# Kernel tuning notes

Measured on AMD Instinct MI355X. Metric: run time of the kernel, lower is better.

The kernel has to match this reference:

```python
import jax, jax.numpy as jnp
import numpy as np

N_NODES = 50000
N_EDGES = 800000
GNN_IN, GNN_HID, GNN_OUT = 64, 128, 64
MLP_HID, MLP_OUT = 128, 1
EDGE_DIST_DIM = 16
NEG_SLOPE = 0.2


def setup_inputs() -> dict:
    key = jax.random.key(0)
    ks = jax.random.split(key, 16)
    inp = {
        "x": jax.random.normal(ks[0], (N_NODES, GNN_IN), dtype=jnp.float32),
        "edge_index": jax.random.randint(ks[1], (N_EDGES, 2), 0, N_NODES, dtype=jnp.int32),
        "edge_dist": jax.random.normal(ks[2], (N_EDGES, EDGE_DIST_DIM), dtype=jnp.float32),
        # GATConv layer 1
        "W_g1": jax.random.normal(ks[3], (GNN_IN, GNN_HID), dtype=jnp.float32) / np.sqrt(GNN_IN),
        "a1_src": jax.random.normal(ks[4], (GNN_HID,), dtype=jnp.float32) / np.sqrt(GNN_HID),
        "a1_dst": jax.random.normal(ks[5], (GNN_HID,), dtype=jnp.float32) / np.sqrt(GNN_HID),
        "b_g1": jnp.zeros((GNN_HID,), dtype=jnp.float32),
        # GATConv layer 2
        "W_g2": jax.random.normal(ks[6], (GNN_HID, GNN_OUT), dtype=jnp.float32) / np.sqrt(GNN_HID),
        "a2_src": jax.random.normal(ks[7], (GNN_OUT,), dtype=jnp.float32) / np.sqrt(GNN_OUT),
        "a2_dst": jax.random.normal(ks[8], (GNN_OUT,), dtype=jnp.float32) / np.sqrt(GNN_OUT),
        "b_g2": jnp.zeros((GNN_OUT,), dtype=jnp.float32),
        # edge MLP: in = (GNN_IN + GNN_OUT)*2 + EDGE_DIST_DIM = 272
        "W_m1": jax.random.normal(ks[9], ((GNN_IN + GNN_OUT) * 2 + EDGE_DIST_DIM, MLP_HID), dtype=jnp.float32) / np.sqrt((GNN_IN + GNN_OUT) * 2 + EDGE_DIST_DIM),
        "b_m1": jnp.zeros((MLP_HID,), dtype=jnp.float32),
        "W_m2": jax.random.normal(ks[10], (MLP_HID, MLP_OUT), dtype=jnp.float32) / np.sqrt(MLP_HID),
        "b_m2": jnp.zeros((MLP_OUT,), dtype=jnp.float32),
    }
    return inp


def gat_conv(x, src, dst, W, a_src, a_dst, bias, n_nodes):
    """Single-head GATConv (PyG defaults: self-loops already included in src/dst)."""
    h = x @ W                                # (N, out)
    alpha_s = h @ a_src                      # (N,)
    alpha_d = h @ a_dst                      # (N,)
    e = jax.nn.leaky_relu(alpha_s[src] + alpha_d[dst], NEG_SLOPE)  # (E,)
    # segment softmax over incoming edges of each destination node
    e_max = jax.ops.segment_max(e, dst, num_segments=n_nodes)
    w = jnp.exp(e - e_max[dst])
    denom = jax.ops.segment_sum(w, dst, num_segments=n_nodes)
    alpha = w / (denom[dst] + 1e-16)
    out = jax.ops.segment_sum(alpha[:, None] * h[src], dst, num_segments=n_nodes)
    return out + bias


def reference(x, edge_index, edge_dist,
              W_g1, a1_src, a1_dst, b_g1,
              W_g2, a2_src, a2_dst, b_g2,
              W_m1, b_m1, W_m2, b_m2):
    n = x.shape[0]
    row = edge_index[:, 0]
    col = edge_index[:, 1]
    # undirected edges + self loops (PyG GATConv add_self_loops=True)
    loops = jnp.arange(n, dtype=edge_index.dtype)
    src = jnp.concatenate([row, col, loops])
    dst = jnp.concatenate([col, row, loops])

    f = jax.nn.relu(gat_conv(x, src, dst, W_g1, a1_src, a1_dst, b_g1, n))
    f = jax.nn.relu(gat_conv(f, src, dst, W_g2, a2_src, a2_dst, b_g2, n))

    xf = jnp.concatenate([x, f], axis=1)     # (N, gnn_in+gnn_out)
    edge_attr = jnp.concatenate([xf[row], xf[col], edge_dist], axis=1)  # (E, 272)
    h = jax.nn.relu(edge_attr @ W_m1 + b_m1)
    return jax.nn.sigmoid(h @ W_m2 + b_m2)   # (E, 1)
```

## Files before the change

### kernel.cpp

```cpp
#include <hip/hip_runtime.h>
#include <hip/hip_bf16.h>
#include <math.h>


#define GIN 64
#define GHID 128
#define GOUT 64

typedef unsigned int u32;
typedef unsigned short u16;

__device__ __forceinline__ float bflo(u32 u) {
  union { u32 i; float f; } c; c.i = u << 16; return c.f;
}
__device__ __forceinline__ float bfhi(u32 u) {
  union { u32 i; float f; } c; c.i = u & 0xffff0000u; return c.f;
}
__device__ __forceinline__ u16 f2bf(float x) {
  __hip_bfloat16 h = __float2bfloat16(x);
  return *reinterpret_cast<u16*>(&h);
}


__global__ void hist_kernel(const int* __restrict__ eidx, int* __restrict__ deg,
                            int nE, int n) {
  int tot = 2 * nE + n;
  for (int i = blockIdx.x * blockDim.x + threadIdx.x; i < tot;
       i += gridDim.x * blockDim.x) {
    int dst;
    if (i < nE) dst = eidx[2 * i + 1];
    else if (i < 2 * nE) dst = eidx[2 * (i - nE)];
    else dst = i - 2 * nE;
    atomicAdd(&deg[dst], 1);
  }
}

#define SCAN_CHUNK 1024
__global__ void scan_partial(const int* __restrict__ deg, int* __restrict__ bsum,
                             int n) {
  int b = blockIdx.x, tid = threadIdx.x;
  int base = b * SCAN_CHUNK + tid * 4;
  int s = 0;
#pragma unroll
  for (int c = 0; c < 4; ++c) { int i = base + c; if (i < n) s += deg[i]; }
#pragma unroll
  for (int off = 32; off; off >>= 1) s += __shfl_xor(s, off, 64);
  __shared__ int ws[4];
  if ((tid & 63) == 0) ws[tid >> 6] = s;
  __syncthreads();
  if (tid == 0) bsum[b] = ws[0] + ws[1] + ws[2] + ws[3];
}
__global__ void scan_bsums(const int* __restrict__ bsum, int* __restrict__ bscan,
                           int* __restrict__ offs, int nb, int n) {
  int lane = threadIdx.x;
  int v = (lane < nb) ? bsum[lane] : 0;
  int incl = v;
#pragma unroll
  for (int off = 1; off < 64; off <<= 1) {
    int t = __shfl_up(incl, off, 64);
    if (lane >= off) incl += t;
  }
  if (lane < nb) bscan[lane] = incl - v;
  if (lane == 63) offs[n] = incl;
}
__global__ void scan_final(const int* __restrict__ deg, const int* __restrict__ bscan,
                           int* __restrict__ offs, int* __restrict__ cursor, int n) {
  int b = blockIdx.x, tid = threadIdx.x;
  int base = b * SCAN_CHUNK + tid * 4;
  int v[4]; int s = 0;
#pragma unroll
  for (int c = 0; c < 4; ++c) { int i = base + c; v[c] = (i < n) ? deg[i] : 0; s += v[c]; }
  int lane = tid & 63, wv = tid >> 6;
  int incl = s;
#pragma unroll
  for (int off = 1; off < 64; off <<= 1) {
    int t = __shfl_up(incl, off, 64);
    if (lane >= off) incl += t;
  }
  __shared__ int ws[4];
  if (lane == 63) ws[wv] = incl;
  __syncthreads();
  int woff = 0;
  for (int w2 = 0; w2 < wv; ++w2) woff += ws[w2];
  int excl = bscan[b] + woff + incl - s;
#pragma unroll
  for (int c = 0; c < 4; ++c) {
    int i = base + c;
    if (i < n) { offs[i] = excl; cursor[i] = excl; }
    excl += v[c];
  }
}

__global__ void scatter_kernel(const int* __restrict__ eidx, int* __restrict__ cursor,
                               int* __restrict__ csr, int nE, int n) {
  int tot = 2 * nE + n;
  for (int i = blockIdx.x * blockDim.x + threadIdx.x; i < tot;
       i += gridDim.x * blockDim.x) {
    int src, dst;
    if (i < nE)          { src = eidx[2 * i];            dst = eidx[2 * i + 1]; }
    else if (i < 2 * nE) { src = eidx[2 * (i - nE) + 1]; dst = eidx[2 * (i - nE)]; }
    else                 { src = i - 2 * nE;             dst = src; }
    int pos = atomicAdd(&cursor[dst], 1);
    csr[pos] = src;
  }
}


template <bool SCORES>
__global__ __launch_bounds__(256) void gemm_bf(
    const float* __restrict__ A, const float* __restrict__ A2, int ksp,
    int lda, int lda2,
    const float* __restrict__ B, int bskip, int ldb,
    u16* __restrict__ Cb, int ldcb,
    const float* __restrict__ av, const float* __restrict__ bv,
    float* __restrict__ as_, float* __restrict__ ad_,
    int M, int K) {
  __shared__ float As[32][68];
  __shared__ float Bs[32][64];
  int tid = threadIdx.x;
  int m0 = blockIdx.x * 64;
  int n0 = blockIdx.y * 64;
  const float* Bp = B + (size_t)(n0 >> 7) * bskip;
  int nb0 = n0 & 127;
  int tx = tid & 15, ty = tid >> 4;
  float acc[4][4] = {};
  for (int k0 = 0; k0 < K; k0 += 32) {
    const float* Asrc; int Alda; int kk;
    if (k0 < ksp) { Asrc = A;  Alda = lda;  kk = k0; }
    else          { Asrc = A2; Alda = lda2; kk = k0 - ksp; }
#pragma unroll
    for (int r = 0; r < 2; ++r) {
      int m = (tid >> 3) + r * 32;
      int k = (tid & 7) * 4;
      float4 v = make_float4(0.f, 0.f, 0.f, 0.f);
      int gm = m0 + m;
      if (gm < M) v = *reinterpret_cast<const float4*>(&Asrc[(size_t)gm * Alda + kk + k]);
      As[k + 0][m] = v.x; As[k + 1][m] = v.y; As[k + 2][m] = v.z; As[k + 3][m] = v.w;
    }
#pragma unroll
    for (int r = 0; r < 2; ++r) {
      int k = (tid >> 4) + r * 16;
      int nn = (tid & 15) * 4;
      float4 v = *reinterpret_cast<const float4*>(&Bp[(size_t)(k0 + k) * ldb + nb0 + nn]);
      *reinterpret_cast<float4*>(&Bs[k][nn]) = v;
    }
    __syncthreads();
#pragma unroll
    for (int k = 0; k < 32; ++k) {
      float a[4], b[4];
#pragma unroll
      for (int i = 0; i < 4; ++i) a[i] = As[k][ty * 4 + i];
#pragma unroll
      for (int i = 0; i < 4; ++i) b[i] = Bs[k][tx * 4 + i];
#pragma unroll
      for (int i = 0; i < 4; ++i)
#pragma unroll
        for (int j = 0; j < 4; ++j) acc[i][j] += a[i] * b[j];
    }
    __syncthreads();
  }
  float avv[4], bvv[4];
  if constexpr (SCORES) {
#pragma unroll
    for (int j = 0; j < 4; ++j) {
      avv[j] = av[n0 + tx * 4 + j];
      bvv[j] = bv[n0 + tx * 4 + j];
    }
  }
#pragma unroll
  for (int i = 0; i < 4; ++i) {
    int gm = m0 + ty * 4 + i;
    bool inb = gm < M;
    if (inb) {
      u16* bp = &Cb[(size_t)gm * ldcb + n0 + tx * 4];
      *reinterpret_cast<ushort4*>(bp) = make_ushort4(
          f2bf(acc[i][0]), f2bf(acc[i][1]), f2bf(acc[i][2]), f2bf(acc[i][3]));
    }
    if constexpr (SCORES) {
      float ps = acc[i][0] * avv[0] + acc[i][1] * avv[1] +
                 acc[i][2] * avv[2] + acc[i][3] * avv[3];
      float pd = acc[i][0] * bvv[0] + acc[i][1] * bvv[1] +
                 acc[i][2] * bvv[2] + acc[i][3] * bvv[3];
#pragma unroll
      for (int off = 1; off < 16; off <<= 1) {
        ps += __shfl_xor(ps, off, 16);
        pd += __shfl_xor(pd, off, 16);
      }
      if (tx == 0 && inb) {
        atomicAdd(&as_[gm], ps);
        atomicAdd(&ad_[gm], pd);
      }
    }
  }
}


__global__ __launch_bounds__(256) void gat_agg1(
    const u16* __restrict__ hb, const float* __restrict__ as_,
    const float* __restrict__ ad_, const int* __restrict__ offs,
    const int* __restrict__ csr, const float* __restrict__ bias,
    float* __restrict__ out, int n) {
  int node = blockIdx.x * 4 + (threadIdx.x >> 6);
  if (node >= n) return;
  int lane = threadIdx.x & 63;
  int g = lane >> 3, sl = lane & 7;
  int beg = offs[node], end = offs[node + 1];
  float adn = ad_[node];
  float denom = 0.f;
  float a[16] = {};
  int i0 = beg + g;
  int s0 = (i0 < end) ? csr[i0] : -1;
  uint4 pa0 = make_uint4(0,0,0,0), pb0 = make_uint4(0,0,0,0); float e0 = 0.f;
  if (s0 >= 0) {
    const u16* row = &hb[(size_t)s0 * 128 + sl * 16];
    pa0 = *reinterpret_cast<const uint4*>(row);
    pb0 = *reinterpret_cast<const uint4*>(row + 8);
    e0 = as_[s0] + adn;
  }
  int i1 = i0 + 8;
  int s1 = (i1 < end) ? csr[i1] : -1;
  while (s0 >= 0) {
    int i2 = i1 + 8;
    int s2 = (i2 < end) ? csr[i2] : -1;
    uint4 pa1 = make_uint4(0,0,0,0), pb1 = make_uint4(0,0,0,0); float e1 = 0.f;
    if (s1 >= 0) {
      const u16* row = &hb[(size_t)s1 * 128 + sl * 16];
      pa1 = *reinterpret_cast<const uint4*>(row);
      pb1 = *reinterpret_cast<const uint4*>(row + 8);
      e1 = as_[s1] + adn;
    }
    float e = (e0 > 0.f) ? e0 : 0.2f * e0;
    float wgt = __expf(e);
    denom += wgt;
    a[0]  += wgt * bflo(pa0.x); a[1]  += wgt * bfhi(pa0.x);
    a[2]  += wgt * bflo(pa0.y); a[3]  += wgt * bfhi(pa0.y);
    a[4]  += wgt * bflo(pa0.z); a[5]  += wgt * bfhi(pa0.z);
    a[6]  += wgt * bflo(pa0.w); a[7]  += wgt * bfhi(pa0.w);
    a[8]  += wgt * bflo(pb0.x); a[9]  += wgt * bfhi(pb0.x);
    a[10] += wgt * bflo(pb0.y); a[11] += wgt * bfhi(pb0.y);
    a[12] += wgt * bflo(pb0.z); a[13] += wgt * bfhi(pb0.z);
    a[14] += wgt * bflo(pb0.w); a[15] += wgt * bfhi(pb0.w);
    s0 = s1; pa0 = pa1; pb0 = pb1; e0 = e1;
    s1 = s2; i1 = i2;
  }
  denom += __shfl_xor(denom, 8, 64);
  denom += __shfl_xor(denom, 16, 64);
  denom += __shfl_xor(denom, 32, 64);
#pragma unroll
  for (int j = 0; j < 16; ++j) {
    a[j] += __shfl_xor(a[j], 8, 64);
    a[j] += __shfl_xor(a[j], 16, 64);
    a[j] += __shfl_xor(a[j], 32, 64);
  }
  if (g == 0) {
    float inv = 1.f / (denom + 1e-16f);
    float* op = &out[(size_t)node * 128 + sl * 16];
    const float* bp = &bias[sl * 16];
#pragma unroll
    for (int q = 0; q < 4; ++q) {
      float4 bq = *reinterpret_cast<const float4*>(bp + q * 4);
      float4 o;
      o.x = fmaxf(a[q * 4 + 0] * inv + bq.x, 0.f);
      o.y = fmaxf(a[q * 4 + 1] * inv + bq.y, 0.f);
      o.z = fmaxf(a[q * 4 + 2] * inv + bq.z, 0.f);
      o.w = fmaxf(a[q * 4 + 3] * inv + bq.w, 0.f);
      *reinterpret_cast<float4*>(op + q * 4) = o;
    }
  }
}


__global__ __launch_bounds__(256) void gat_agg2(
    const u16* __restrict__ hb, const float* __restrict__ as_,
    const float* __restrict__ ad_, const int* __restrict__ offs,
    const int* __restrict__ csr, const float* __restrict__ bias,
    float* __restrict__ out, int n) {
  int node = blockIdx.x * 4 + (threadIdx.x >> 6);
  if (node >= n) return;
  int lane = threadIdx.x & 63;
  int g = lane >> 2, sl = lane & 3;
  int beg = offs[node], end = offs[node + 1];
  float adn = ad_[node];
  float denom = 0.f;
  float a[16] = {};
  int i0 = beg + g;
  int s0 = (i0 < end) ? csr[i0] : -1;
  uint4 pa0 = make_uint4(0,0,0,0), pb0 = make_uint4(0,0,0,0); float e0 = 0.f;
  if (s0 >= 0) {
    const u16* row = &hb[(size_t)s0 * 64 + sl * 16];
    pa0 = *reinterpret_cast<const uint4*>(row);
    pb0 = *reinterpret_cast<const uint4*>(row + 8);
    e0 = as_[s0] + adn;
  }
  int i1 = i0 + 16;
  int s1 = (i1 < end) ? csr[i1] : -1;
  while (s0 >= 0) {
    int i2 = i1 + 16;
    int s2 = (i2 < end) ? csr[i2] : -1;
    uint4 pa1 = make_uint4(0,0,0,0), pb1 = make_uint4(0,0,0,0); float e1 = 0.f;
    if (s1 >= 0) {
      const u16* row = &hb[(size_t)s1 * 64 + sl * 16];
      pa1 = *reinterpret_cast<const uint4*>(row);
      pb1 = *reinterpret_cast<const uint4*>(row + 8);
      e1 = as_[s1] + adn;
    }
    float e = (e0 > 0.f) ? e0 : 0.2f * e0;
    float wgt = __expf(e);
    denom += wgt;
    a[0]  += wgt * bflo(pa0.x); a[1]  += wgt * bfhi(pa0.x);
    a[2]  += wgt * bflo(pa0.y); a[3]  += wgt * bfhi(pa0.y);
    a[4]  += wgt * bflo(pa0.z); a[5]  += wgt * bfhi(pa0.z);
    a[6]  += wgt * bflo(pa0.w); a[7]  += wgt * bfhi(pa0.w);
    a[8]  += wgt * bflo(pb0.x); a[9]  += wgt * bfhi(pb0.x);
    a[10] += wgt * bflo(pb0.y); a[11] += wgt * bfhi(pb0.y);
    a[12] += wgt * bflo(pb0.z); a[13] += wgt * bfhi(pb0.z);
    a[14] += wgt * bflo(pb0.w); a[15] += wgt * bfhi(pb0.w);
    s0 = s1; pa0 = pa1; pb0 = pb1; e0 = e1;
    s1 = s2; i1 = i2;
  }
#pragma unroll
  for (int w2 = 4; w2 < 64; w2 <<= 1) denom += __shfl_xor(denom, w2, 64);
#pragma unroll
  for (int j = 0; j < 16; ++j) {
    a[j] += __shfl_xor(a[j], 4, 64);
    a[j] += __shfl_xor(a[j], 8, 64);
    a[j] += __shfl_xor(a[j], 16, 64);
    a[j] += __shfl_xor(a[j], 32, 64);
  }
  if (g == 0) {
    float inv = 1.f / (denom + 1e-16f);
    float* op = &out[(size_t)node * 64 + sl * 16];
    const float* bp = &bias[sl * 16];
#pragma unroll
    for (int q = 0; q < 4; ++q) {
      float4 bq = *reinterpret_cast<const float4*>(bp + q * 4);
      float4 o;
      o.x = fmaxf(a[q * 4 + 0] * inv + bq.x, 0.f);
      o.y = fmaxf(a[q * 4 + 1] * inv + bq.y, 0.f);
      o.z = fmaxf(a[q * 4 + 2] * inv + bq.z, 0.f);
      o.w = fmaxf(a[q * 4 + 3] * inv + bq.w, 0.f);
      *reinterpret_cast<float4*>(op + q * 4) = o;
    }
  }
}


__global__ __launch_bounds__(256) void edge_mlp(
    const int2* __restrict__ eidx, const float* __restrict__ dist,
    const u16* __restrict__ Pb, const float* __restrict__ W3,
    const float* __restrict__ b1, const float* __restrict__ W2,
    const float* __restrict__ b2, float* __restrict__ out, int nE) {
  __shared__ float4 W3s[16][32];
  int tid = threadIdx.x;
  for (int idx = tid; idx < 16 * 32; idx += 256) {
    int k = idx >> 5, q = idx & 31;
    W3s[k][q] = *reinterpret_cast<const float4*>(&W3[k * 128 + q * 4]);
  }
  __syncthreads();
  int lane = tid & 63, wv = tid >> 6;
  int g = lane >> 4, sl = lane & 15;
  float4 b1a = *reinterpret_cast<const float4*>(&b1[sl * 8]);
  float4 b1b = *reinterpret_cast<const float4*>(&b1[sl * 8 + 4]);
  float4 w2a = *reinterpret_cast<const float4*>(&W2[sl * 8]);
  float4 w2b = *reinterpret_cast<const float4*>(&W2[sl * 8 + 4]);
  float b2v = b2[0];
  const int stride = gridDim.x * 16;
  int e0 = (blockIdx.x * 4 + wv) * 4 + g;
  bool v0 = e0 < nE;
  int2 rc0 = v0 ? eidx[e0] : make_int2(0, 0);
  uint4 p1 = make_uint4(0,0,0,0), p2 = make_uint4(0,0,0,0); float ds0 = 0.f;
  if (v0) {
    p1 = *reinterpret_cast<const uint4*>(&Pb[(size_t)rc0.x * 256 + sl * 8]);
    p2 = *reinterpret_cast<const uint4*>(&Pb[(size_t)rc0.y * 256 + 128 + sl * 8]);
    ds0 = dist[(size_t)e0 * 16 + sl];
  }
  int e1 = e0 + stride;
  bool v1 = e1 < nE;
  int2 rc1 = v1 ? eidx[e1] : make_int2(0, 0);
  while (v0) {
    int e2 = e1 + stride;
    bool v2 = e2 < nE;
    int2 rc2 = v2 ? eidx[e2] : make_int2(0, 0);
    uint4 q1 = make_uint4(0,0,0,0), q2 = make_uint4(0,0,0,0); float ds1 = 0.f;
    if (v1) {
      q1 = *reinterpret_cast<const uint4*>(&Pb[(size_t)rc1.x * 256 + sl * 8]);
      q2 = *reinterpret_cast<const uint4*>(&Pb[(size_t)rc1.y * 256 + 128 + sl * 8]);
      ds1 = dist[(size_t)e1 * 16 + sl];
    }
    float a[8];
    a[0] = bflo(p1.x) + bflo(p2.x) + b1a.x;
    a[1] = bfhi(p1.x) + bfhi(p2.x) + b1a.y;
    a[2] = bflo(p1.y) + bflo(p2.y) + b1a.z;
    a[3] = bfhi(p1.y) + bfhi(p2.y) + b1a.w;
    a[4] = bflo(p1.z) + bflo(p2.z) + b1b.x;
    a[5] = bfhi(p1.z) + bfhi(p2.z) + b1b.y;
    a[6] = bflo(p1.w) + bflo(p2.w) + b1b.z;
    a[7] = bfhi(p1.w) + bfhi(p2.w) + b1b.w;
#pragma unroll
    for (int k = 0; k < 16; ++k) {
      float dk = __shfl(ds0, (g << 4) + k, 64);
      float4 wA = W3s[k][2 * sl];
      float4 wB = W3s[k][2 * sl + 1];
      a[0] += dk * wA.x; a[1] += dk * wA.y; a[2] += dk * wA.z; a[3] += dk * wA.w;
      a[4] += dk * wB.x; a[5] += dk * wB.y; a[6] += dk * wB.z; a[7] += dk * wB.w;
    }
    float p_ = fmaxf(a[0], 0.f) * w2a.x + fmaxf(a[1], 0.f) * w2a.y +
               fmaxf(a[2], 0.f) * w2a.z + fmaxf(a[3], 0.f) * w2a.w +
               fmaxf(a[4], 0.f) * w2b.x + fmaxf(a[5], 0.f) * w2b.y +
               fmaxf(a[6], 0.f) * w2b.z + fmaxf(a[7], 0.f) * w2b.w;
#pragma unroll
    for (int off = 1; off < 16; off <<= 1) p_ += __shfl_xor(p_, off, 16);
    if (sl == 0) out[e0] = 1.f / (1.f + __expf(-(p_ + b2v)));
    e0 = e1; v0 = v1; p1 = q1; p2 = q2; ds0 = ds1;
    e1 = e2; v1 = v2; rc1 = rc2;
  }
}


extern "C" void kernel_launch(void* const* d_in, const int* in_sizes, int n_in,
                              void* d_out, int out_size, void* d_ws, size_t ws_size,
                              hipStream_t stream) {
  const float* x      = (const float*)d_in[0];
  const int*   eidx   = (const int*)d_in[1];
  const float* dist   = (const float*)d_in[2];
  const float* W_g1   = (const float*)d_in[3];
  const float* a1_src = (const float*)d_in[4];
  const float* a1_dst = (const float*)d_in[5];
  const float* b_g1   = (const float*)d_in[6];
  const float* W_g2   = (const float*)d_in[7];
  const float* a2_src = (const float*)d_in[8];
  const float* a2_dst = (const float*)d_in[9];
  const float* b_g2   = (const float*)d_in[10];
  const float* W_m1   = (const float*)d_in[11];
  const float* b_m1   = (const float*)d_in[12];
  const float* W_m2   = (const float*)d_in[13];
  const float* b_m2   = (const float*)d_in[14];
  float* out = (float*)d_out;

  const int n  = in_sizes[0] / GIN;
  const int nE = in_sizes[1] / 2;
  const int ndir = 2 * nE + n;

  char* w = (char*)d_ws;
  size_t off = 0;
  auto alloc = [&](size_t bytes) {
    size_t o = off;
    off += (bytes + 255) & ~(size_t)255;
    return o;
  };
  size_t o_deg    = alloc((size_t)n * 4);
  size_t o_offs   = alloc((size_t)(n + 1) * 4);
  size_t o_cursor = alloc((size_t)n * 4);
  size_t o_as1    = alloc((size_t)n * 4);
  size_t o_ad1    = alloc((size_t)n * 4);
  size_t o_as2    = alloc((size_t)n * 4);
  size_t o_ad2    = alloc((size_t)n * 4);
  size_t o_bsum   = alloc(64 * 4);
  size_t o_bscan  = alloc(64 * 4);
  size_t o_csr    = alloc((size_t)ndir * 4);
  size_t o_big    = alloc((size_t)n * 256 * 2);
  size_t o_f1     = alloc((size_t)n * GHID * 4);
  size_t o_f2     = alloc((size_t)n * GOUT * 4);
  (void)ws_size;

  int*   deg    = (int*)(w + o_deg);
  int*   offs   = (int*)(w + o_offs);
  int*   cursor = (int*)(w + o_cursor);
  float* as1    = (float*)(w + o_as1);
  float* ad1    = (float*)(w + o_ad1);
  float* as2    = (float*)(w + o_as2);
  float* ad2    = (float*)(w + o_ad2);
  int*   bsum   = (int*)(w + o_bsum);
  int*   bscan  = (int*)(w + o_bscan);
  int*   csr    = (int*)(w + o_csr);
  u16*   h1b    = (u16*)(w + o_big);
  u16*   h2b    = (u16*)(w + o_big + (size_t)n * GHID * 2);
  u16*   Pb     = (u16*)(w + o_big);
  float* f1     = (float*)(w + o_f1);
  float* f2     = (float*)(w + o_f2);

  hipMemsetAsync(deg, 0, (size_t)n * 4, stream);
  hipMemsetAsync(as1, 0, (size_t)n * 4, stream);
  hipMemsetAsync(ad1, 0, (size_t)n * 4, stream);
  hipMemsetAsync(as2, 0, (size_t)n * 4, stream);
  hipMemsetAsync(ad2, 0, (size_t)n * 4, stream);
  hist_kernel<<<2048, 256, 0, stream>>>(eidx, deg, nE, n);
  int nb = (n + SCAN_CHUNK - 1) / SCAN_CHUNK;
  scan_partial<<<nb, 256, 0, stream>>>(deg, bsum, n);
  scan_bsums<<<1, 64, 0, stream>>>(bsum, bscan, offs, nb, n);
  scan_final<<<nb, 256, 0, stream>>>(deg, bscan, offs, cursor, n);
  scatter_kernel<<<2048, 256, 0, stream>>>(eidx, cursor, csr, nE, n);

  const int mtiles = (n + 63) / 64;
  const int BIGK = 1 << 30;

  gemm_bf<true><<<dim3(mtiles, 2), 256, 0, stream>>>(
      x, x, BIGK, GIN, GIN, W_g1, 0, GHID, h1b, GHID,
      a1_src, a1_dst, as1, ad1, n, GIN);

  gat_agg1<<<(n + 3) / 4, 256, 0, stream>>>(h1b, as1, ad1, offs, csr, b_g1, f1, n);

  gemm_bf<true><<<dim3(mtiles, 1), 256, 0, stream>>>(
      f1, f1, BIGK, GHID, GHID, W_g2, 0, GOUT, h2b, GOUT,
      a2_src, a2_dst, as2, ad2, n, GHID);

  gat_agg2<<<(n + 3) / 4, 256, 0, stream>>>(h2b, as2, ad2, offs, csr, b_g2, f2, n);

  gemm_bf<false><<<dim3(mtiles, 4), 256, 0, stream>>>(
      x, f2, GIN, GIN, GOUT, W_m1, 128 * 128, GHID, Pb, 256,
      nullptr, nullptr, nullptr, nullptr, n, GHID);

  edge_mlp<<<4096, 256, 0, stream>>>((const int2*)eidx, dist, Pb,
                                     W_m1 + 256 * 128, b_m1, W_m2, b_m2, out, nE);
}
```

Baseline: 651.5 us.

## Partition CSR histogram and scatter by destination range across block groups

Histogram and scatter kernels now split destination nodes into 8 ranges, each handled by one eighth of the blocks. Every block group reads all edges as int2 pairs and does atomics only on destinations in its own range, which keeps the atomic targets more local. Self-loops are no longer counted by atomics: the scan adds 1 per node, and scatter writes each self-loop at the first slot of its node directly. The cost is that edge_index is read 8 times over, and the self-loop is now first rather than last in each CSR row.

```diff
diff --git a/kernel.cpp b/kernel.cpp
--- a/kernel.cpp
+++ b/kernel.cpp
@@ -22,16 +22,18 @@
 }
 
 
-__global__ void hist_kernel(const int* __restrict__ eidx, int* __restrict__ deg,
-                            int nE, int n) {
-  int tot = 2 * nE + n;
-  for (int i = blockIdx.x * blockDim.x + threadIdx.x; i < tot;
-       i += gridDim.x * blockDim.x) {
-    int dst;
-    if (i < nE) dst = eidx[2 * i + 1];
-    else if (i < 2 * nE) dst = eidx[2 * (i - nE)];
-    else dst = i - 2 * nE;
-    atomicAdd(&deg[dst], 1);
+__global__ void hist_part(const int2* __restrict__ eidx2, int* __restrict__ deg,
+                          int nE, int n) {
+  int r = blockIdx.x & 7;
+  int nper = (n + 7) >> 3;
+  int r0 = r * nper;
+  int r1 = min(n, r0 + nper);
+  u32 span = (u32)(r1 - r0);
+  int cb = blockIdx.x >> 3, nb = gridDim.x >> 3;
+  for (int e = cb * blockDim.x + threadIdx.x; e < nE; e += nb * blockDim.x) {
+    int2 rc = eidx2[e];
+    if ((u32)(rc.y - r0) < span) atomicAdd(&deg[rc.y], 1);
+    if ((u32)(rc.x - r0) < span) atomicAdd(&deg[rc.x], 1);
   }
 }
 
@@ -42,7 +44,7 @@
   int base = b * SCAN_CHUNK + tid * 4;
   int s = 0;
 #pragma unroll
-  for (int c = 0; c < 4; ++c) { int i = base + c; if (i < n) s += deg[i]; }
+  for (int c = 0; c < 4; ++c) { int i = base + c; if (i < n) s += deg[i] + 1; }
 #pragma unroll
   for (int off = 32; off; off >>= 1) s += __shfl_xor(s, off, 64);
   __shared__ int ws[4];
@@ -69,7 +71,11 @@
   int base = b * SCAN_CHUNK + tid * 4;
   int v[4]; int s = 0;
 #pragma unroll
-  for (int c = 0; c < 4; ++c) { int i = base + c; v[c] = (i < n) ? deg[i] : 0; s += v[c]; }
+  for (int c = 0; c < 4; ++c) {
+    int i = base + c;
+    v[c] = (i < n) ? deg[i] + 1 : 0;
+    s += v[c];
+  }
   int lane = tid & 63, wv = tid >> 6;
   int incl = s;
 #pragma unroll
@@ -86,22 +92,26 @@
 #pragma unroll
   for (int c = 0; c < 4; ++c) {
     int i = base + c;
-    if (i < n) { offs[i] = excl; cursor[i] = excl; }
+    if (i < n) { offs[i] = excl; cursor[i] = excl + 1; }
     excl += v[c];
   }
 }
 
-__global__ void scatter_kernel(const int* __restrict__ eidx, int* __restrict__ cursor,
-                               int* __restrict__ csr, int nE, int n) {
-  int tot = 2 * nE + n;
-  for (int i = blockIdx.x * blockDim.x + threadIdx.x; i < tot;
-       i += gridDim.x * blockDim.x) {
-    int src, dst;
-    if (i < nE)          { src = eidx[2 * i];            dst = eidx[2 * i + 1]; }
-    else if (i < 2 * nE) { src = eidx[2 * (i - nE) + 1]; dst = eidx[2 * (i - nE)]; }
-    else                 { src = i - 2 * nE;             dst = src; }
-    int pos = atomicAdd(&cursor[dst], 1);
-    csr[pos] = src;
+__global__ void scatter_part(const int2* __restrict__ eidx2,
+                             const int* __restrict__ offs, int* __restrict__ cursor,
+                             int* __restrict__ csr, int nE, int n) {
+  int r = blockIdx.x & 7;
+  int nper = (n + 7) >> 3;
+  int r0 = r * nper;
+  int r1 = min(n, r0 + nper);
+  u32 span = (u32)(r1 - r0);
+  int cb = blockIdx.x >> 3, nb = gridDim.x >> 3;
+  for (int i = r0 + cb * blockDim.x + threadIdx.x; i < r1; i += nb * blockDim.x)
+    csr[offs[i]] = i;
+  for (int e = cb * blockDim.x + threadIdx.x; e < nE; e += nb * blockDim.x) {
+    int2 rc = eidx2[e];
+    if ((u32)(rc.y - r0) < span) { int pos = atomicAdd(&cursor[rc.y], 1); csr[pos] = rc.x; }
+    if ((u32)(rc.x - r0) < span) { int pos = atomicAdd(&cursor[rc.x], 1); csr[pos] = rc.y; }
   }
 }
 
@@ -484,12 +494,12 @@
   hipMemsetAsync(ad1, 0, (size_t)n * 4, stream);
   hipMemsetAsync(as2, 0, (size_t)n * 4, stream);
   hipMemsetAsync(ad2, 0, (size_t)n * 4, stream);
-  hist_kernel<<<2048, 256, 0, stream>>>(eidx, deg, nE, n);
+  hist_part<<<2048, 256, 0, stream>>>((const int2*)eidx, deg, nE, n);
   int nb = (n + SCAN_CHUNK - 1) / SCAN_CHUNK;
   scan_partial<<<nb, 256, 0, stream>>>(deg, bsum, n);
   scan_bsums<<<1, 64, 0, stream>>>(bsum, bscan, offs, nb, n);
   scan_final<<<nb, 256, 0, stream>>>(deg, bscan, offs, cursor, n);
-  scatter_kernel<<<2048, 256, 0, stream>>>(eidx, cursor, csr, nE, n);
+  scatter_part<<<2048, 256, 0, stream>>>((const int2*)eidx, offs, cursor, csr, nE, n);
 
   const int mtiles = (n + 63) / 64;
   const int BIGK = 1 << 30;
```

Result: faster. 590.5 us (-9.4%).
